# Kernel tuning notes

Measured on AMD Instinct MI355X. Metric: run time of the kernel, lower is better.

Reference implementation:

```python
import jax, jax.numpy as jnp
import numpy as np

B, T, D, H, NH = 128, 64, 64, 128, 4


def setup_inputs() -> dict:
    key = jax.random.key(0)
    ks = jax.random.split(key, 32)
    s = 0.05
    inp = {
        "x": jax.random.normal(ks[0], (B, T, D), dtype=jnp.float32),
        "mask": jnp.ones((B, T), dtype=jnp.int32),
        # per-feature GRU params (input size 1, PyTorch gate order r,z,n)
        "Wih": jax.random.normal(ks[1], (D, 3 * H), dtype=jnp.float32) * s,
        "Whh": jax.random.normal(ks[2], (D, 3 * H, H), dtype=jnp.float32) * s,
        "bih": jax.random.normal(ks[3], (D, 3 * H), dtype=jnp.float32) * s,
        "bhh": jax.random.normal(ks[4], (D, 3 * H), dtype=jnp.float32) * s,
        # MHA projections (stored [in,out]; y = x @ W + b)
        "Wq": jax.random.normal(ks[5], (H, H), dtype=jnp.float32) * s,
        "bq": jnp.zeros((H,), dtype=jnp.float32),
        "Wk": jax.random.normal(ks[6], (H, H), dtype=jnp.float32) * s,
        "bk": jnp.zeros((H,), dtype=jnp.float32),
        "Wv": jax.random.normal(ks[7], (H, H), dtype=jnp.float32) * s,
        "bv": jnp.zeros((H,), dtype=jnp.float32),
        "Wo": jax.random.normal(ks[8], (H, H), dtype=jnp.float32) * s,
        "bo": jnp.zeros((H,), dtype=jnp.float32),
        # FFN
        "W1": jax.random.normal(ks[9], (H, 2 * H), dtype=jnp.float32) * s,
        "b1": jnp.zeros((2 * H,), dtype=jnp.float32),
        "W2": jax.random.normal(ks[10], (2 * H, H), dtype=jnp.float32) * s,
        "b2": jnp.zeros((H,), dtype=jnp.float32),
        # LayerNorms
        "g1": jnp.ones((H,), dtype=jnp.float32),
        "be1": jnp.zeros((H,), dtype=jnp.float32),
        "g2": jnp.ones((H,), dtype=jnp.float32),
        "be2": jnp.zeros((H,), dtype=jnp.float32),
        # FinalAttentionQKV
        "Fq": jax.random.normal(ks[11], (H, H), dtype=jnp.float32) * s,
        "fbq": jnp.zeros((H,), dtype=jnp.float32),
        "Fk": jax.random.normal(ks[12], (H, H), dtype=jnp.float32) * s,
        "fbk": jnp.zeros((H,), dtype=jnp.float32),
        "Fv": jax.random.normal(ks[13], (H, H), dtype=jnp.float32) * s,
        "fbv": jnp.zeros((H,), dtype=jnp.float32),
        "Fout": jax.random.normal(ks[14], (H,), dtype=jnp.float32) * s,
        "fbout": jnp.zeros((), dtype=jnp.float32),
    }
    return inp


def _layernorm(x, g, b, eps=1e-5):
    m = jnp.mean(x, axis=-1, keepdims=True)
    v = jnp.mean((x - m) ** 2, axis=-1, keepdims=True)
    return (x - m) * jax.lax.rsqrt(v + eps) * g + b


def _forward(x, mask, Wih, Whh, bih, bhh, Wq, bq, Wk, bk, Wv, bv, Wo, bo,
             W1, b1, W2, b2, g1, be1, g2, be2,
             Fq, fbq, Fk, fbk, Fv, fbv, Fout, fbout):
    Bc, Tc, Dc = x.shape
    Hc = Whh.shape[-1]

    # --- D independent GRUs, fused: batch axes (B, D), scalar input per step ---
    def step(h, xt):  # h: [B,D,H], xt: [B,D]
        gx = xt[..., None] * Wih + bih                     # [B,D,3H]
        gh = jnp.einsum('bdh,dkh->bdk', h, Whh) + bhh      # [B,D,3H]
        r = jax.nn.sigmoid(gx[..., :Hc] + gh[..., :Hc])
        z = jax.nn.sigmoid(gx[..., Hc:2 * Hc] + gh[..., Hc:2 * Hc])
        n = jnp.tanh(gx[..., 2 * Hc:] + r * gh[..., 2 * Hc:])
        hn = (1.0 - z) * n + z * h
        return hn, hn

    xs = jnp.transpose(x, (1, 0, 2))                        # [T,B,D]
    h0 = jnp.zeros((Bc, Dc, Hc), dtype=x.dtype)
    _, ys = jax.lax.scan(step, h0, xs)                      # [T,B,D,H]

    # last_by_lengths: gather hidden state at index lengths-1 per batch element
    lengths = jnp.sum(mask, axis=1)                         # [B]
    idx = jnp.clip(lengths - 1, 0, Tc - 1)
    emb = ys[idx, jnp.arange(Bc)]                           # [B,D,H] (D tokens)

    # --- MHA (self-attention over D feature tokens); dropout = identity (eval) ---
    dk = Hc // NH
    def split_heads(t):
        return jnp.transpose(t.reshape(Bc, Dc, NH, dk), (0, 2, 1, 3))  # [B,NH,D,dk]
    q = split_heads(emb @ Wq + bq)
    k = split_heads(emb @ Wk + bk)
    v = split_heads(emb @ Wv + bv)
    scores = jnp.einsum('bhnd,bhmd->bhnm', q, k) / jnp.sqrt(jnp.float32(dk))
    attn = jax.nn.softmax(scores, axis=-1)
    o = jnp.einsum('bhnm,bhmd->bhnd', attn, v)
    o = jnp.transpose(o, (0, 2, 1, 3)).reshape(Bc, Dc, Hc)
    mha_out = o @ Wo + bo

    h1 = _layernorm(emb + mha_out, g1, be1)
    ffn = jax.nn.relu(h1 @ W1 + b1) @ W2 + b2
    h2 = _layernorm(h1 + ffn, g2, be2)

    # --- FinalAttentionQKV ---
    fq = (h2[:, -1, :] @ Fq + fbq)[:, None, :]              # [B,1,H]
    fk = h2 @ Fk + fbk                                      # [B,D,H]
    fv = h2 @ Fv + fbv                                      # [B,D,H]
    e = jnp.tanh(fq + fk) @ Fout + fbout                    # [B,D]
    a = jax.nn.softmax(e, axis=-1)
    return jnp.einsum('bn,bnh->bh', a, fv)                  # [B,H]


def reference(x, mask, Wih, Whh, bih, bhh, Wq, bq, Wk, bk, Wv, bv, Wo, bo,
              W1, b1, W2, b2, g1, be1, g2, be2,
              Fq, fbq, Fk, fbk, Fv, fbv, Fout, fbout):
    return _forward(x, mask, Wih, Whh, bih, bhh, Wq, bq, Wk, bk, Wv, bv, Wo, bo,
                    W1, b1, W2, b2, g1, be1, g2, be2,
                    Fq, fbq, Fk, fbk, Fv, fbv, Fout, fbout)
```

## Files before the change

### kernel.cpp

```cpp
#include <hip/hip_runtime.h>
#include <math.h>

#define BB 128
#define TT 64
#define DD 64
#define HH 128
#define NHH 4
#define K3H 384

typedef __attribute__((ext_vector_type(8))) short short8_t;
typedef __attribute__((ext_vector_type(4))) float float4_t;

#define LOG2E 1.4426950408889634f

__device__ __forceinline__ unsigned short f2bf(float f) {
    unsigned int u = __float_as_uint(f);
    u += 0x7fffu + ((u >> 16) & 1u);
    return (unsigned short)(u >> 16);
}

__device__ __forceinline__ unsigned pack_bf2(float lo, float hi) {
    return (unsigned)f2bf(lo) | ((unsigned)f2bf(hi) << 16);
}

__device__ __forceinline__ float bf2f(unsigned short s) {
    return __uint_as_float((unsigned)s << 16);
}

__global__ __launch_bounds__(512, 4) void gru_mfma_kernel(
    const float* __restrict__ x, const int* __restrict__ mask,
    const float* __restrict__ Wih, const float* __restrict__ Whh,
    const float* __restrict__ bih, const float* __restrict__ bhh,
    float* __restrict__ emb)
{
    const int d  = blockIdx.x;
    const int b0 = blockIdx.y * 16;
    const int tid = threadIdx.x;
    const int w = tid >> 6;
    const int l = tid & 63;
    const int m = l & 15;
    const int q = l >> 4;

    __shared__ __align__(16) unsigned short hbuf[2][16][136];
    __shared__ float xs_t[TT][16];
    __shared__ int tstar_s[16];

    for (int idx = tid; idx < 16 * TT; idx += 512) {
        int t = idx >> 4, row = idx & 15;
        xs_t[t][row] = x[((size_t)(b0 + row) * TT + t) * DD + d];
    }
    if (tid < 16) {
        int b = b0 + tid, len = 0;
        for (int t = 0; t < TT; ++t) len += mask[b * TT + t];
        int ts = len - 1;
        if (ts < 0) ts = 0;
        if (ts > TT - 1) ts = TT - 1;
        tstar_s[tid] = ts;
    }
    for (int idx = tid; idx < 16 * 136; idx += 512)
        ((unsigned short*)hbuf)[idx] = 0;

    short8_t Wf[3][4];
#pragma unroll
    for (int g = 0; g < 3; ++g) {
        float sc = (g == 2) ? (2.f * LOG2E) : (-LOG2E);
        int kcol = g * HH + 16 * w + m;
        const float* wrow = Whh + ((size_t)d * K3H + kcol) * HH;
#pragma unroll
        for (int kc = 0; kc < 4; ++kc) {
            int j0 = kc * 32 + q * 8;
            float4 w0 = *(const float4*)(wrow + j0);
            float4 w1 = *(const float4*)(wrow + j0 + 4);
            short8_t f;
            f[0] = (short)f2bf(w0.x * sc); f[1] = (short)f2bf(w0.y * sc);
            f[2] = (short)f2bf(w0.z * sc); f[3] = (short)f2bf(w0.w * sc);
            f[4] = (short)f2bf(w1.x * sc); f[5] = (short)f2bf(w1.y * sc);
            f[6] = (short)f2bf(w1.z * sc); f[7] = (short)f2bf(w1.w * sc);
            Wf[g][kc] = f;
        }
    }

    const int hcol0 = 16 * w + q * 4;
    float4 wr4 = *(const float4*)&Wih[d * K3H + hcol0];
    float4 wz4 = *(const float4*)&Wih[d * K3H + HH + hcol0];
    float4 wn4 = *(const float4*)&Wih[d * K3H + 2 * HH + hcol0];
    float4 br4 = *(const float4*)&bih[d * K3H + hcol0];
    float4 bz4 = *(const float4*)&bih[d * K3H + HH + hcol0];
    float4 bni4 = *(const float4*)&bih[d * K3H + 2 * HH + hcol0];
    float4 bhr4 = *(const float4*)&bhh[d * K3H + hcol0];
    float4 bhz4 = *(const float4*)&bhh[d * K3H + HH + hcol0];
    float4 bnh4 = *(const float4*)&bhh[d * K3H + 2 * HH + hcol0];
    float brs[4], bzs[4], bnis[4], bnhs[4], wrs[4], wzs[4], wns[4];
#pragma unroll
    for (int r = 0; r < 4; ++r) {
        wrs[r] = -LOG2E * ((const float*)&wr4)[r];
        wzs[r] = -LOG2E * ((const float*)&wz4)[r];
        wns[r] = 2.f * LOG2E * ((const float*)&wn4)[r];
        brs[r] = -LOG2E * (((const float*)&br4)[r] + ((const float*)&bhr4)[r]);
        bzs[r] = -LOG2E * (((const float*)&bz4)[r] + ((const float*)&bhz4)[r]);
        bnis[r] = 2.f * LOG2E * ((const float*)&bni4)[r];
        bnhs[r] = 2.f * LOG2E * ((const float*)&bnh4)[r];
    }

    float hprev[4];
#pragma unroll
    for (int i = 0; i < 4; ++i) hprev[i] = 0.f;

    __syncthreads();
    const int tstar_m = tstar_s[m];
    float* embp = emb + (((size_t)(b0 + m)) * DD + d) * HH + hcol0;

    for (int t = 0; t < TT; ++t) {
        const unsigned short* hb = &hbuf[t & 1][0][0];
        unsigned short* hbn = &hbuf[(t & 1) ^ 1][0][0];

        short8_t hf[4];
#pragma unroll
        for (int kc = 0; kc < 4; ++kc)
            hf[kc] = *(const short8_t*)(hb + m * 136 + kc * 32 + q * 8);
        float xv = xs_t[t][m];

        float4_t ar = {0.f,0.f,0.f,0.f}, az = {0.f,0.f,0.f,0.f}, an = {0.f,0.f,0.f,0.f};
#pragma unroll
        for (int kc = 0; kc < 4; ++kc) {
            ar = __builtin_amdgcn_mfma_f32_16x16x32_bf16(Wf[0][kc], hf[kc], ar, 0, 0, 0);
            az = __builtin_amdgcn_mfma_f32_16x16x32_bf16(Wf[1][kc], hf[kc], az, 0, 0, 0);
            an = __builtin_amdgcn_mfma_f32_16x16x32_bf16(Wf[2][kc], hf[kc], an, 0, 0, 0);
        }

        float hn4[4];
#pragma unroll
        for (int reg = 0; reg < 4; ++reg) {
            float grs = ar[reg] + fmaf(xv, wrs[reg], brs[reg]);
            float gzs = az[reg] + fmaf(xv, wzs[reg], bzs[reg]);
            float rg = __builtin_amdgcn_rcpf(1.f + __builtin_amdgcn_exp2f(grs));
            float zg = __builtin_amdgcn_rcpf(1.f + __builtin_amdgcn_exp2f(gzs));
            float gns = fmaf(rg, an[reg] + bnhs[reg], fmaf(xv, wns[reg], bnis[reg]));
            float tn = fmaf(-2.f, __builtin_amdgcn_rcpf(__builtin_amdgcn_exp2f(gns) + 1.f), 1.f);
            float hn = fmaf(zg, hprev[reg] - tn, tn);
            hprev[reg] = hn;
            hn4[reg] = hn;
        }
        uint2 uu;
        uu.x = pack_bf2(hn4[0], hn4[1]);
        uu.y = pack_bf2(hn4[2], hn4[3]);
        *(uint2*)(hbn + m * 136 + hcol0) = uu;
        if (t == tstar_m) {
            float4 hv; hv.x = hn4[0]; hv.y = hn4[1]; hv.z = hn4[2]; hv.w = hn4[3];
            *(float4*)embp = hv;
        }
        __syncthreads();
    }
}


__device__ __forceinline__ void load_wfrag(const float* __restrict__ Wp, int N,
                                           int col, float scale, int q,
                                           short8_t fr[4])
{
#pragma unroll
    for (int kc = 0; kc < 4; ++kc) {
        const float* p = Wp + (size_t)(kc * 32 + q * 8) * N + col;
        short8_t f;
#pragma unroll
        for (int j = 0; j < 8; ++j)
            f[j] = (short)f2bf(p[(size_t)j * N] * scale);
        fr[kc] = f;
    }
}

__device__ __forceinline__ void load_afrag(const unsigned short (*S)[136],
                                           short8_t Af[4][4], int m16, int q)
{
#pragma unroll
    for (int mt = 0; mt < 4; ++mt)
#pragma unroll
        for (int kc = 0; kc < 4; ++kc)
            Af[mt][kc] = *(const short8_t*)&S[mt * 16 + m16][kc * 32 + q * 8];
}

__device__ __forceinline__ void mm_regw(short8_t Af[4][4], short8_t Bf[4],
                                        float4_t acc[4])
{
#pragma unroll
    for (int mt = 0; mt < 4; ++mt) {
        float4_t a = acc[mt];
#pragma unroll
        for (int kc = 0; kc < 4; ++kc)
            a = __builtin_amdgcn_mfma_f32_16x16x32_bf16(Af[mt][kc], Bf[kc], a, 0, 0, 0);
        acc[mt] = a;
    }
}

__device__ __forceinline__ void zero4(float4_t acc[4]) {
#pragma unroll
    for (int mt = 0; mt < 4; ++mt) acc[mt] = (float4_t){0.f, 0.f, 0.f, 0.f};
}

__device__ __forceinline__ void store_rows(unsigned short (*Dst)[136], float4_t acc[4],
                                           float bv, int relu, int col, int q)
{
#pragma unroll
    for (int mt = 0; mt < 4; ++mt)
#pragma unroll
        for (int reg = 0; reg < 4; ++reg) {
            float v = acc[mt][reg] + bv;
            if (relu) v = fmaxf(v, 0.f);
            Dst[mt * 16 + q * 4 + reg][col] = f2bf(v);
        }
}

__global__ __launch_bounds__(512) void tail_kernel(
    const float* __restrict__ emb,
    const float* __restrict__ Wq, const float* __restrict__ bq,
    const float* __restrict__ Wk, const float* __restrict__ bk,
    const float* __restrict__ Wv, const float* __restrict__ bv,
    const float* __restrict__ Wo, const float* __restrict__ bo,
    const float* __restrict__ W1, const float* __restrict__ b1,
    const float* __restrict__ W2, const float* __restrict__ b2,
    const float* __restrict__ g1, const float* __restrict__ be1,
    const float* __restrict__ g2, const float* __restrict__ be2,
    const float* __restrict__ Fq, const float* __restrict__ fbq,
    const float* __restrict__ Fk, const float* __restrict__ fbk,
    const float* __restrict__ Fv, const float* __restrict__ fbv,
    const float* __restrict__ Fout, const float* __restrict__ fbout,
    float* __restrict__ out)
{
    const int b = blockIdx.x;
    const int tid = threadIdx.x;
    const int w = tid >> 6, l = tid & 63, m16 = l & 15, q = l >> 4;
    const int col = w * 16 + m16;

    __shared__ __align__(16) unsigned short E[64][136];
    __shared__ __align__(16) unsigned short Qs[64][136];
    __shared__ __align__(16) unsigned short Ks[64][136];
    __shared__ __align__(16) unsigned short Vt[128][72];
    __shared__ float sc4[4][64][66];
    __shared__ float lnp[64][8], lnp2[64][8];
    __shared__ float mean_s[64], rs_s[64];
    __shared__ float fq_s[128], fo_s[128], e_s[64], red_s[256];

    const float* embB = emb + (size_t)b * 64 * 128;
    const float SS = 0.17677669529663687f;

    short8_t WqF[4], WkF[4], WvF[4];
    load_wfrag(Wq, 128, col, SS, q, WqF);
    load_wfrag(Wk, 128, col, 1.f, q, WkF);
    load_wfrag(Wv, 128, col, 1.f, q, WvF);
    float bqv = bq[col] * SS, bkv = bk[col], bvv = bv[col];

    for (int it = tid; it < 2048; it += 512) {
        int r = it >> 5, c4 = (it & 31) << 2;
        float4 a = *(const float4*)&embB[r * 128 + c4];
        uint2 p; p.x = pack_bf2(a.x, a.y); p.y = pack_bf2(a.z, a.w);
        *(uint2*)&E[r][c4] = p;
    }
    __syncthreads();

    short8_t Af[4][4];
    float4_t acc[4];
    load_afrag(E, Af, m16, q);

    zero4(acc); mm_regw(Af, WqF, acc); store_rows(Qs, acc, bqv, 0, col, q);
    zero4(acc); mm_regw(Af, WkF, acc); store_rows(Ks, acc, bkv, 0, col, q);
    zero4(acc); mm_regw(Af, WvF, acc);
#pragma unroll
    for (int mt = 0; mt < 4; ++mt) {
        uint2 pk;
        pk.x = pack_bf2(acc[mt][0] + bvv, acc[mt][1] + bvv);
        pk.y = pack_bf2(acc[mt][2] + bvv, acc[mt][3] + bvv);
        *(uint2*)&Vt[col][mt * 16 + q * 4] = pk;
    }
    __syncthreads();

    short8_t WoF[4], W1aF[4], W1bF[4];
    load_wfrag(Wo, 128, col, 1.f, q, WoF);
    load_wfrag(W1, 256, col, 1.f, q, W1aF);
    load_wfrag(W1, 256, 128 + col, 1.f, q, W1bF);
    float bov = bo[col], b1a = b1[col], b1b = b1[128 + col];
    float g1v = g1[col], be1v = be1[col];

    {
        int hd = w >> 1, ntb = (w & 1) * 2;
#pragma unroll
        for (int mt = 0; mt < 4; ++mt) {
            short8_t Aq = *(const short8_t*)&Qs[mt * 16 + m16][hd * 32 + q * 8];
#pragma unroll
            for (int nn = 0; nn < 2; ++nn) {
                int nt = ntb + nn;
                short8_t Bk = *(const short8_t*)&Ks[nt * 16 + m16][hd * 32 + q * 8];
                float4_t a = {0.f, 0.f, 0.f, 0.f};
                a = __builtin_amdgcn_mfma_f32_16x16x32_bf16(Aq, Bk, a, 0, 0, 0);
#pragma unroll
                for (int reg = 0; reg < 4; ++reg)
                    sc4[hd][mt * 16 + q * 4 + reg][nt * 16 + m16] = a[reg];
            }
        }
    }
    __syncthreads();

    {
        int pr = tid >> 1, hd2 = pr >> 6, row = pr & 63, half = (tid & 1) * 32;
        float v[32]; float mx = -1e30f;
#pragma unroll
        for (int c = 0; c < 32; ++c) { v[c] = sc4[hd2][row][half + c]; mx = fmaxf(mx, v[c]); }
        mx = fmaxf(mx, __shfl_xor(mx, 1));
        float sum = 0.f;
#pragma unroll
        for (int c = 0; c < 32; ++c) { v[c] = __expf(v[c] - mx); sum += v[c]; }
        sum += __shfl_xor(sum, 1);
        float inv = __builtin_amdgcn_rcpf(sum);
        unsigned short (*Pd)[136] = (hd2 < 2) ? Qs : Ks;
        int cb = (hd2 & 1) * 64 + half;
#pragma unroll
        for (int c = 0; c < 16; ++c)
            *(unsigned*)&Pd[row][cb + 2 * c] = pack_bf2(v[2 * c] * inv, v[2 * c + 1] * inv);
    }
    __syncthreads();

    {
        int hd = w >> 1, nt = w & 1;
        const unsigned short (*P)[136] = (hd < 2) ? (const unsigned short (*)[136])Qs
                                                  : (const unsigned short (*)[136])Ks;
        int pb = (hd & 1) * 64;
        int vrow = hd * 32 + nt * 16 + m16;
        short8_t B0f = *(const short8_t*)&Vt[vrow][q * 8];
        short8_t B1f = *(const short8_t*)&Vt[vrow][32 + q * 8];
#pragma unroll
        for (int mt = 0; mt < 4; ++mt) {
            short8_t A0 = *(const short8_t*)&P[mt * 16 + m16][pb + q * 8];
            short8_t A1 = *(const short8_t*)&P[mt * 16 + m16][pb + 32 + q * 8];
            float4_t a = {0.f, 0.f, 0.f, 0.f};
            a = __builtin_amdgcn_mfma_f32_16x16x32_bf16(A0, B0f, a, 0, 0, 0);
            a = __builtin_amdgcn_mfma_f32_16x16x32_bf16(A1, B1f, a, 0, 0, 0);
#pragma unroll
            for (int reg = 0; reg < 4; ++reg)
                E[mt * 16 + q * 4 + reg][vrow] = f2bf(a[reg]);
        }
    }
    __syncthreads();

    short8_t W2aF[4], W2bF[4], FkF[4], FvF[4];
    load_wfrag(W2, 128, col, 1.f, q, W2aF);
    load_wfrag(W2 + (size_t)128 * 128, 128, col, 1.f, q, W2bF);
    load_wfrag(Fk, 128, col, 1.f, q, FkF);
    load_wfrag(Fv, 128, col, 1.f, q, FvF);
    float b2v = b2[col], fbkv = fbk[col], fbvv = fbv[col];
    float g2v = g2[col], be2v = be2[col];

    load_afrag(E, Af, m16, q);
    zero4(acc); mm_regw(Af, WoF, acc);
    float h1v[4][4];
#pragma unroll
    for (int mt = 0; mt < 4; ++mt)
#pragma unroll
        for (int reg = 0; reg < 4; ++reg) {
            int row = mt * 16 + q * 4 + reg;
            h1v[mt][reg] = acc[mt][reg] + bov + embB[(size_t)row * 128 + col];
        }
#pragma unroll
    for (int mt = 0; mt < 4; ++mt)
#pragma unroll
        for (int reg = 0; reg < 4; ++reg) {
            float s = h1v[mt][reg], s2 = s * s;
            s += __shfl_xor(s, 1); s += __shfl_xor(s, 2); s += __shfl_xor(s, 4); s += __shfl_xor(s, 8);
            s2 += __shfl_xor(s2, 1); s2 += __shfl_xor(s2, 2); s2 += __shfl_xor(s2, 4); s2 += __shfl_xor(s2, 8);
            if (m16 == 0) { int row = mt * 16 + q * 4 + reg; lnp[row][w] = s; lnp2[row][w] = s2; }
        }
    __syncthreads();
    if (tid < 64) {
        float s = 0.f, s2 = 0.f;
#pragma unroll
        for (int k = 0; k < 8; ++k) { s += lnp[tid][k]; s2 += lnp2[tid][k]; }
        float mn = s * (1.f / 128.f);
        mean_s[tid] = mn;
        rs_s[tid] = rsqrtf(s2 * (1.f / 128.f) - mn * mn + 1e-5f);
    }
    __syncthreads();
#pragma unroll
    for (int mt = 0; mt < 4; ++mt)
#pragma unroll
        for (int reg = 0; reg < 4; ++reg) {
            int row = mt * 16 + q * 4 + reg;
            float hv = (h1v[mt][reg] - mean_s[row]) * rs_s[row] * g1v + be1v;
            h1v[mt][reg] = hv;
            E[row][col] = f2bf(hv);
        }
    __syncthreads();

    load_afrag(E, Af, m16, q);
    zero4(acc); mm_regw(Af, W1aF, acc); store_rows(Qs, acc, b1a, 1, col, q);
    zero4(acc); mm_regw(Af, W1bF, acc); store_rows(Ks, acc, b1b, 1, col, q);
    __syncthreads();

    {
        short8_t AfQ[4][4], AfK[4][4];
        load_afrag(Qs, AfQ, m16, q);
        load_afrag(Ks, AfK, m16, q);
        zero4(acc); mm_regw(AfQ, W2aF, acc); mm_regw(AfK, W2bF, acc);
    }
#pragma unroll
    for (int mt = 0; mt < 4; ++mt)
#pragma unroll
        for (int reg = 0; reg < 4; ++reg)
            h1v[mt][reg] = acc[mt][reg] + b2v + h1v[mt][reg];
#pragma unroll
    for (int mt = 0; mt < 4; ++mt)
#pragma unroll
        for (int reg = 0; reg < 4; ++reg) {
            float s = h1v[mt][reg], s2 = s * s;
            s += __shfl_xor(s, 1); s += __shfl_xor(s, 2); s += __shfl_xor(s, 4); s += __shfl_xor(s, 8);
            s2 += __shfl_xor(s2, 1); s2 += __shfl_xor(s2, 2); s2 += __shfl_xor(s2, 4); s2 += __shfl_xor(s2, 8);
            if (m16 == 0) { int row = mt * 16 + q * 4 + reg; lnp[row][w] = s; lnp2[row][w] = s2; }
        }
    __syncthreads();
    if (tid < 64) {
        float s = 0.f, s2 = 0.f;
#pragma unroll
        for (int k = 0; k < 8; ++k) { s += lnp[tid][k]; s2 += lnp2[tid][k]; }
        float mn = s * (1.f / 128.f);
        mean_s[tid] = mn;
        rs_s[tid] = rsqrtf(s2 * (1.f / 128.f) - mn * mn + 1e-5f);
    }
    __syncthreads();
#pragma unroll
    for (int mt = 0; mt < 4; ++mt)
#pragma unroll
        for (int reg = 0; reg < 4; ++reg) {
            int row = mt * 16 + q * 4 + reg;
            float hv = (h1v[mt][reg] - mean_s[row]) * rs_s[row] * g2v + be2v;
            E[row][col] = f2bf(hv);
        }
    __syncthreads();

    load_afrag(E, Af, m16, q);
    zero4(acc); mm_regw(Af, FkF, acc); store_rows(Qs, acc, fbkv, 0, col, q);
    zero4(acc); mm_regw(Af, FvF, acc); store_rows(Ks, acc, fbvv, 0, col, q);
    if (tid < 128) {
        fo_s[tid] = Fout[tid];
        float a = fbq[tid];
        for (int mm2 = 0; mm2 < 128; ++mm2)
            a = fmaf(bf2f(E[63][mm2]), Fq[mm2 * 128 + tid], a);
        fq_s[tid] = a;
    }
    __syncthreads();

    {
        int dd = tid >> 3, c8 = tid & 7;
        float p = 0.f;
#pragma unroll
        for (int c = 0; c < 16; ++c) {
            int cc = c8 * 16 + c;
            float t = fq_s[cc] + bf2f(Qs[dd][cc]);
            float tn = 1.f - 2.f * __builtin_amdgcn_rcpf(
                __builtin_amdgcn_exp2f(2.f * LOG2E * t) + 1.f);
            p = fmaf(tn, fo_s[cc], p);
        }
        p += __shfl_xor(p, 1); p += __shfl_xor(p, 2); p += __shfl_xor(p, 4);
        if (c8 == 0) e_s[dd] = p + fbout[0];
    }
    __syncthreads();
    if (tid < 64) {
        float e = e_s[tid], mx = e;
        for (int o = 32; o; o >>= 1) mx = fmaxf(mx, __shfl_xor(mx, o));
        float pe = __expf(e - mx);
        float s = pe;
        for (int o = 32; o; o >>= 1) s += __shfl_xor(s, o);
        e_s[tid] = pe / s;
    }
    __syncthreads();
    if (tid < 256) {
        int c2 = tid & 127, rg2 = tid >> 7;
        float a = 0.f;
        for (int d2 = rg2 * 32; d2 < rg2 * 32 + 32; ++d2)
            a = fmaf(e_s[d2], bf2f(Ks[d2][c2]), a);
        red_s[tid] = a;
    }
    __syncthreads();
    if (tid < 128)
        out[(size_t)b * 128 + tid] = red_s[tid] + red_s[tid + 128];
}

extern "C" void kernel_launch(void* const* d_in, const int* in_sizes, int n_in,
                              void* d_out, int out_size, void* d_ws, size_t ws_size,
                              hipStream_t stream)
{
    const float* x    = (const float*)d_in[0];
    const int*   mask = (const int*)d_in[1];
    const float* Wih  = (const float*)d_in[2];
    const float* Whh  = (const float*)d_in[3];
    const float* bih  = (const float*)d_in[4];
    const float* bhh  = (const float*)d_in[5];
    const float* Wq = (const float*)d_in[6];   const float* bq = (const float*)d_in[7];
    const float* Wk = (const float*)d_in[8];   const float* bk = (const float*)d_in[9];
    const float* Wv = (const float*)d_in[10];  const float* bv = (const float*)d_in[11];
    const float* Wo = (const float*)d_in[12];  const float* bo = (const float*)d_in[13];
    const float* W1 = (const float*)d_in[14];  const float* b1 = (const float*)d_in[15];
    const float* W2 = (const float*)d_in[16];  const float* b2 = (const float*)d_in[17];
    const float* g1 = (const float*)d_in[18];  const float* be1 = (const float*)d_in[19];
    const float* g2 = (const float*)d_in[20];  const float* be2 = (const float*)d_in[21];
    const float* Fq = (const float*)d_in[22];  const float* fbq = (const float*)d_in[23];
    const float* Fk = (const float*)d_in[24];  const float* fbk = (const float*)d_in[25];
    const float* Fv = (const float*)d_in[26];  const float* fbv = (const float*)d_in[27];
    const float* Fout = (const float*)d_in[28]; const float* fbout = (const float*)d_in[29];
    float* out = (float*)d_out;
    float* ws  = (float*)d_ws;

    float* emb = ws;

    gru_mfma_kernel<<<dim3(DD, BB / 16), 512, 0, stream>>>(x, mask, Wih, Whh, bih, bhh, emb);
    tail_kernel<<<BB, 512, 0, stream>>>(
        emb, Wq, bq, Wk, bk, Wv, bv, Wo, bo, W1, b1, W2, b2,
        g1, be1, g2, be2, Fq, fbq, Fk, fbk, Fv, fbv, Fout, fbout, out);
}
```

Measured before the change: 250.9 us.

## Split tail kernel across two blocks per batch and add final reduce kernel

The tail kernel now runs two blocks per batch element. Each block recomputes K and V for all 64 rows but handles Q, attention, Wo, FFN, LayerNorms and the Fk/Fv projections for only its 32 rows. Fk, Fv and the last-row Fq projection go to workspace, and a new third kernel computes the final tanh-attention softmax and weighted sum. The GRU loop also seeds the MFMA accumulators with the hidden-path biases and uses the hardware bf16 pack intrinsic. This doubles the tail's parallelism and cuts shared memory per block, at the cost of redundant K/V work, global round-trips and an extra launch.

```diff
diff --git a/kernel.cpp b/kernel.cpp
--- a/kernel.cpp
+++ b/kernel.cpp
@@ -1,4 +1,5 @@
 #include <hip/hip_runtime.h>
+#include <hip/hip_bf16.h>
 #include <math.h>
 
 #define BB 128
@@ -21,6 +22,13 @@
 
 __device__ __forceinline__ unsigned pack_bf2(float lo, float hi) {
     return (unsigned)f2bf(lo) | ((unsigned)f2bf(hi) << 16);
+}
+
+__device__ __forceinline__ unsigned pack_bf2_hw(float lo, float hi) {
+    __hip_bfloat162 p = __float22bfloat162_rn(make_float2(lo, hi));
+    unsigned u;
+    __builtin_memcpy(&u, &p, 4);
+    return u;
 }
 
 __device__ __forceinline__ float bf2f(unsigned short s) {
@@ -120,7 +128,9 @@
             hf[kc] = *(const short8_t*)(hb + m * 136 + kc * 32 + q * 8);
         float xv = xs_t[t][m];
 
-        float4_t ar = {0.f,0.f,0.f,0.f}, az = {0.f,0.f,0.f,0.f}, an = {0.f,0.f,0.f,0.f};
+        float4_t ar = {brs[0], brs[1], brs[2], brs[3]};
+        float4_t az = {bzs[0], bzs[1], bzs[2], bzs[3]};
+        float4_t an = {bnhs[0], bnhs[1], bnhs[2], bnhs[3]};
 #pragma unroll
         for (int kc = 0; kc < 4; ++kc) {
             ar = __builtin_amdgcn_mfma_f32_16x16x32_bf16(Wf[0][kc], hf[kc], ar, 0, 0, 0);
@@ -131,19 +141,19 @@
         float hn4[4];
 #pragma unroll
         for (int reg = 0; reg < 4; ++reg) {
-            float grs = ar[reg] + fmaf(xv, wrs[reg], brs[reg]);
-            float gzs = az[reg] + fmaf(xv, wzs[reg], bzs[reg]);
+            float grs = fmaf(xv, wrs[reg], ar[reg]);
+            float gzs = fmaf(xv, wzs[reg], az[reg]);
             float rg = __builtin_amdgcn_rcpf(1.f + __builtin_amdgcn_exp2f(grs));
             float zg = __builtin_amdgcn_rcpf(1.f + __builtin_amdgcn_exp2f(gzs));
-            float gns = fmaf(rg, an[reg] + bnhs[reg], fmaf(xv, wns[reg], bnis[reg]));
+            float gns = fmaf(rg, an[reg], fmaf(xv, wns[reg], bnis[reg]));
             float tn = fmaf(-2.f, __builtin_amdgcn_rcpf(__builtin_amdgcn_exp2f(gns) + 1.f), 1.f);
             float hn = fmaf(zg, hprev[reg] - tn, tn);
             hprev[reg] = hn;
             hn4[reg] = hn;
         }
         uint2 uu;
-        uu.x = pack_bf2(hn4[0], hn4[1]);
-        uu.y = pack_bf2(hn4[2], hn4[3]);
+        uu.x = pack_bf2_hw(hn4[0], hn4[1]);
+        uu.y = pack_bf2_hw(hn4[2], hn4[3]);
         *(uint2*)(hbn + m * 136 + hcol0) = uu;
         if (t == tstar_m) {
             float4 hv; hv.x = hn4[0]; hv.y = hn4[1]; hv.z = hn4[2]; hv.w = hn4[3];
@@ -167,47 +177,6 @@
             f[j] = (short)f2bf(p[(size_t)j * N] * scale);
         fr[kc] = f;
     }
-}
-
-__device__ __forceinline__ void load_afrag(const unsigned short (*S)[136],
-                                           short8_t Af[4][4], int m16, int q)
-{
-#pragma unroll
-    for (int mt = 0; mt < 4; ++mt)
-#pragma unroll
-        for (int kc = 0; kc < 4; ++kc)
-            Af[mt][kc] = *(const short8_t*)&S[mt * 16 + m16][kc * 32 + q * 8];
-}
-
-__device__ __forceinline__ void mm_regw(short8_t Af[4][4], short8_t Bf[4],
-                                        float4_t acc[4])
-{
-#pragma unroll
-    for (int mt = 0; mt < 4; ++mt) {
-        float4_t a = acc[mt];
-#pragma unroll
-        for (int kc = 0; kc < 4; ++kc)
-            a = __builtin_amdgcn_mfma_f32_16x16x32_bf16(Af[mt][kc], Bf[kc], a, 0, 0, 0);
-        acc[mt] = a;
-    }
-}
-
-__device__ __forceinline__ void zero4(float4_t acc[4]) {
-#pragma unroll
-    for (int mt = 0; mt < 4; ++mt) acc[mt] = (float4_t){0.f, 0.f, 0.f, 0.f};
-}
-
-__device__ __forceinline__ void store_rows(unsigned short (*Dst)[136], float4_t acc[4],
-                                           float bv, int relu, int col, int q)
-{
-#pragma unroll
-    for (int mt = 0; mt < 4; ++mt)
-#pragma unroll
-        for (int reg = 0; reg < 4; ++reg) {
-            float v = acc[mt][reg] + bv;
-            if (relu) v = fmaxf(v, 0.f);
-            Dst[mt * 16 + q * 4 + reg][col] = f2bf(v);
-        }
 }
 
 __global__ __launch_bounds__(512) void tail_kernel(
@@ -223,10 +192,11 @@
     const float* __restrict__ Fq, const float* __restrict__ fbq,
     const float* __restrict__ Fk, const float* __restrict__ fbk,
     const float* __restrict__ Fv, const float* __restrict__ fbv,
-    const float* __restrict__ Fout, const float* __restrict__ fbout,
-    float* __restrict__ out)
+    float* __restrict__ fkb, float* __restrict__ fvb, float* __restrict__ fqb)
 {
-    const int b = blockIdx.x;
+    const int b = blockIdx.x >> 1;
+    const int half = blockIdx.x & 1;
+    const int r0 = half * 32;
     const int tid = threadIdx.x;
     const int w = tid >> 6, l = tid & 63, m16 = l & 15, q = l >> 4;
     const int col = w * 16 + m16;
@@ -235,10 +205,9 @@
     __shared__ __align__(16) unsigned short Qs[64][136];
     __shared__ __align__(16) unsigned short Ks[64][136];
     __shared__ __align__(16) unsigned short Vt[128][72];
-    __shared__ float sc4[4][64][66];
-    __shared__ float lnp[64][8], lnp2[64][8];
-    __shared__ float mean_s[64], rs_s[64];
-    __shared__ float fq_s[128], fo_s[128], e_s[64], red_s[256];
+    __shared__ float sc4[4][32][66];
+    __shared__ float lnp[32][8], lnp2[32][8];
+    __shared__ float mean_s[32], rs_s[32];
 
     const float* embB = emb + (size_t)b * 64 * 128;
     const float SS = 0.17677669529663687f;
@@ -257,19 +226,49 @@
     }
     __syncthreads();
 
-    short8_t Af[4][4];
-    float4_t acc[4];
-    load_afrag(E, Af, m16, q);
-
-    zero4(acc); mm_regw(Af, WqF, acc); store_rows(Qs, acc, bqv, 0, col, q);
-    zero4(acc); mm_regw(Af, WkF, acc); store_rows(Ks, acc, bkv, 0, col, q);
-    zero4(acc); mm_regw(Af, WvF, acc);
-#pragma unroll
-    for (int mt = 0; mt < 4; ++mt) {
-        uint2 pk;
-        pk.x = pack_bf2(acc[mt][0] + bvv, acc[mt][1] + bvv);
-        pk.y = pack_bf2(acc[mt][2] + bvv, acc[mt][3] + bvv);
-        *(uint2*)&Vt[col][mt * 16 + q * 4] = pk;
+    short8_t Af4[4][4];
+#pragma unroll
+    for (int mt = 0; mt < 4; ++mt)
+#pragma unroll
+        for (int kc = 0; kc < 4; ++kc)
+            Af4[mt][kc] = *(const short8_t*)&E[mt * 16 + m16][kc * 32 + q * 8];
+
+    {
+        float4_t a4[4];
+#pragma unroll
+        for (int mt = 0; mt < 4; ++mt) {
+            float4_t a = {0.f, 0.f, 0.f, 0.f};
+#pragma unroll
+            for (int kc = 0; kc < 4; ++kc)
+                a = __builtin_amdgcn_mfma_f32_16x16x32_bf16(Af4[mt][kc], WkF[kc], a, 0, 0, 0);
+            a4[mt] = a;
+        }
+#pragma unroll
+        for (int mt = 0; mt < 4; ++mt)
+#pragma unroll
+            for (int reg = 0; reg < 4; ++reg)
+                Ks[mt * 16 + q * 4 + reg][col] = f2bf(a4[mt][reg] + bkv);
+#pragma unroll
+        for (int mt = 0; mt < 4; ++mt) {
+            float4_t a = {0.f, 0.f, 0.f, 0.f};
+#pragma unroll
+            for (int kc = 0; kc < 4; ++kc)
+                a = __builtin_amdgcn_mfma_f32_16x16x32_bf16(Af4[mt][kc], WvF[kc], a, 0, 0, 0);
+            uint2 pk;
+            pk.x = pack_bf2(a[0] + bvv, a[1] + bvv);
+            pk.y = pack_bf2(a[2] + bvv, a[3] + bvv);
+            *(uint2*)&Vt[col][mt * 16 + q * 4] = pk;
+        }
+#pragma unroll
+        for (int mt = 0; mt < 2; ++mt) {
+            float4_t a = {0.f, 0.f, 0.f, 0.f};
+#pragma unroll
+            for (int kc = 0; kc < 4; ++kc)
+                a = __builtin_amdgcn_mfma_f32_16x16x32_bf16(Af4[half * 2 + mt][kc], WqF[kc], a, 0, 0, 0);
+#pragma unroll
+            for (int reg = 0; reg < 4; ++reg)
+                Qs[r0 + mt * 16 + q * 4 + reg][col] = f2bf(a[reg] + bqv);
+        }
     }
     __syncthreads();
 
@@ -283,8 +282,8 @@
     {
         int hd = w >> 1, ntb = (w & 1) * 2;
 #pragma unroll
-        for (int mt = 0; mt < 4; ++mt) {
-            short8_t Aq = *(const short8_t*)&Qs[mt * 16 + m16][hd * 32 + q * 8];
+        for (int mt = 0; mt < 2; ++mt) {
+            short8_t Aq = *(const short8_t*)&Qs[r0 + mt * 16 + m16][hd * 32 + q * 8];
 #pragma unroll
             for (int nn = 0; nn < 2; ++nn) {
                 int nt = ntb + nn;
@@ -300,42 +299,41 @@
     __syncthreads();
 
     {
-        int pr = tid >> 1, hd2 = pr >> 6, row = pr & 63, half = (tid & 1) * 32;
-        float v[32]; float mx = -1e30f;
-#pragma unroll
-        for (int c = 0; c < 32; ++c) { v[c] = sc4[hd2][row][half + c]; mx = fmaxf(mx, v[c]); }
+        int pr = tid >> 2, sub = tid & 3;
+        int hd2 = pr >> 5, row = pr & 31;
+        float v[16]; float mx = -1e30f;
+#pragma unroll
+        for (int c = 0; c < 16; ++c) { v[c] = sc4[hd2][row][sub * 16 + c]; mx = fmaxf(mx, v[c]); }
         mx = fmaxf(mx, __shfl_xor(mx, 1));
+        mx = fmaxf(mx, __shfl_xor(mx, 2));
         float sum = 0.f;
 #pragma unroll
-        for (int c = 0; c < 32; ++c) { v[c] = __expf(v[c] - mx); sum += v[c]; }
-        sum += __shfl_xor(sum, 1);
+        for (int c = 0; c < 16; ++c) { v[c] = __expf(v[c] - mx); sum += v[c]; }
+        sum += __shfl_xor(sum, 1); sum += __shfl_xor(sum, 2);
         float inv = __builtin_amdgcn_rcpf(sum);
-        unsigned short (*Pd)[136] = (hd2 < 2) ? Qs : Ks;
-        int cb = (hd2 & 1) * 64 + half;
-#pragma unroll
-        for (int c = 0; c < 16; ++c)
-            *(unsigned*)&Pd[row][cb + 2 * c] = pack_bf2(v[2 * c] * inv, v[2 * c + 1] * inv);
+        int prow = (hd2 >> 1) * 32 + row, pc = (hd2 & 1) * 64 + sub * 16;
+#pragma unroll
+        for (int c = 0; c < 8; ++c)
+            *(unsigned*)&Qs[prow][pc + 2 * c] = pack_bf2(v[2 * c] * inv, v[2 * c + 1] * inv);
     }
     __syncthreads();
 
     {
-        int hd = w >> 1, nt = w & 1;
-        const unsigned short (*P)[136] = (hd < 2) ? (const unsigned short (*)[136])Qs
-                                                  : (const unsigned short (*)[136])Ks;
-        int pb = (hd & 1) * 64;
-        int vrow = hd * 32 + nt * 16 + m16;
+        int hd = w >> 1, ntv = w & 1;
+        int vrow = hd * 32 + ntv * 16 + m16;
         short8_t B0f = *(const short8_t*)&Vt[vrow][q * 8];
         short8_t B1f = *(const short8_t*)&Vt[vrow][32 + q * 8];
-#pragma unroll
-        for (int mt = 0; mt < 4; ++mt) {
-            short8_t A0 = *(const short8_t*)&P[mt * 16 + m16][pb + q * 8];
-            short8_t A1 = *(const short8_t*)&P[mt * 16 + m16][pb + 32 + q * 8];
+        int prow0 = (hd >> 1) * 32, pc = (hd & 1) * 64;
+#pragma unroll
+        for (int mt = 0; mt < 2; ++mt) {
+            short8_t A0 = *(const short8_t*)&Qs[prow0 + mt * 16 + m16][pc + q * 8];
+            short8_t A1 = *(const short8_t*)&Qs[prow0 + mt * 16 + m16][pc + 32 + q * 8];
             float4_t a = {0.f, 0.f, 0.f, 0.f};
             a = __builtin_amdgcn_mfma_f32_16x16x32_bf16(A0, B0f, a, 0, 0, 0);
             a = __builtin_amdgcn_mfma_f32_16x16x32_bf16(A1, B1f, a, 0, 0, 0);
 #pragma unroll
             for (int reg = 0; reg < 4; ++reg)
-                E[mt * 16 + q * 4 + reg][vrow] = f2bf(a[reg]);
+                E[r0 + mt * 16 + q * 4 + reg][vrow] = f2bf(a[reg]);
         }
     }
     __syncthreads();
@@ -348,27 +346,36 @@
     float b2v = b2[col], fbkv = fbk[col], fbvv = fbv[col];
     float g2v = g2[col], be2v = be2[col];
 
-    load_afrag(E, Af, m16, q);
-    zero4(acc); mm_regw(Af, WoF, acc);
-    float h1v[4][4];
-#pragma unroll
-    for (int mt = 0; mt < 4; ++mt)
-#pragma unroll
-        for (int reg = 0; reg < 4; ++reg) {
-            int row = mt * 16 + q * 4 + reg;
-            h1v[mt][reg] = acc[mt][reg] + bov + embB[(size_t)row * 128 + col];
-        }
-#pragma unroll
-    for (int mt = 0; mt < 4; ++mt)
+    short8_t Af2[2][4];
+#pragma unroll
+    for (int mt = 0; mt < 2; ++mt)
+#pragma unroll
+        for (int kc = 0; kc < 4; ++kc)
+            Af2[mt][kc] = *(const short8_t*)&E[r0 + mt * 16 + m16][kc * 32 + q * 8];
+    float h1v[2][4];
+#pragma unroll
+    for (int mt = 0; mt < 2; ++mt) {
+        float4_t a = {0.f, 0.f, 0.f, 0.f};
+#pragma unroll
+        for (int kc = 0; kc < 4; ++kc)
+            a = __builtin_amdgcn_mfma_f32_16x16x32_bf16(Af2[mt][kc], WoF[kc], a, 0, 0, 0);
+#pragma unroll
+        for (int reg = 0; reg < 4; ++reg) {
+            int row = r0 + mt * 16 + q * 4 + reg;
+            h1v[mt][reg] = a[reg] + bov + embB[(size_t)row * 128 + col];
+        }
+    }
+#pragma unroll
+    for (int mt = 0; mt < 2; ++mt)
 #pragma unroll
         for (int reg = 0; reg < 4; ++reg) {
             float s = h1v[mt][reg], s2 = s * s;
             s += __shfl_xor(s, 1); s += __shfl_xor(s, 2); s += __shfl_xor(s, 4); s += __shfl_xor(s, 8);
             s2 += __shfl_xor(s2, 1); s2 += __shfl_xor(s2, 2); s2 += __shfl_xor(s2, 4); s2 += __shfl_xor(s2, 8);
-            if (m16 == 0) { int row = mt * 16 + q * 4 + reg; lnp[row][w] = s; lnp2[row][w] = s2; }
-        }
-    __syncthreads();
-    if (tid < 64) {
+            if (m16 == 0) { int lr = mt * 16 + q * 4 + reg; lnp[lr][w] = s; lnp2[lr][w] = s2; }
+        }
+    __syncthreads();
+    if (tid < 32) {
         float s = 0.f, s2 = 0.f;
 #pragma unroll
         for (int k = 0; k < 8; ++k) { s += lnp[tid][k]; s2 += lnp2[tid][k]; }
@@ -378,43 +385,66 @@
     }
     __syncthreads();
 #pragma unroll
-    for (int mt = 0; mt < 4; ++mt)
-#pragma unroll
-        for (int reg = 0; reg < 4; ++reg) {
-            int row = mt * 16 + q * 4 + reg;
-            float hv = (h1v[mt][reg] - mean_s[row]) * rs_s[row] * g1v + be1v;
+    for (int mt = 0; mt < 2; ++mt)
+#pragma unroll
+        for (int reg = 0; reg < 4; ++reg) {
+            int lr = mt * 16 + q * 4 + reg;
+            float hv = (h1v[mt][reg] - mean_s[lr]) * rs_s[lr] * g1v + be1v;
             h1v[mt][reg] = hv;
-            E[row][col] = f2bf(hv);
-        }
-    __syncthreads();
-
-    load_afrag(E, Af, m16, q);
-    zero4(acc); mm_regw(Af, W1aF, acc); store_rows(Qs, acc, b1a, 1, col, q);
-    zero4(acc); mm_regw(Af, W1bF, acc); store_rows(Ks, acc, b1b, 1, col, q);
-    __syncthreads();
-
-    {
-        short8_t AfQ[4][4], AfK[4][4];
-        load_afrag(Qs, AfQ, m16, q);
-        load_afrag(Ks, AfK, m16, q);
-        zero4(acc); mm_regw(AfQ, W2aF, acc); mm_regw(AfK, W2bF, acc);
-    }
-#pragma unroll
-    for (int mt = 0; mt < 4; ++mt)
+            E[r0 + lr][col] = f2bf(hv);
+        }
+    __syncthreads();
+
+#pragma unroll
+    for (int mt = 0; mt < 2; ++mt)
+#pragma unroll
+        for (int kc = 0; kc < 4; ++kc)
+            Af2[mt][kc] = *(const short8_t*)&E[r0 + mt * 16 + m16][kc * 32 + q * 8];
+#pragma unroll
+    for (int mt = 0; mt < 2; ++mt) {
+        float4_t a = {0.f, 0.f, 0.f, 0.f}, c2 = {0.f, 0.f, 0.f, 0.f};
+#pragma unroll
+        for (int kc = 0; kc < 4; ++kc) {
+            a  = __builtin_amdgcn_mfma_f32_16x16x32_bf16(Af2[mt][kc], W1aF[kc], a, 0, 0, 0);
+            c2 = __builtin_amdgcn_mfma_f32_16x16x32_bf16(Af2[mt][kc], W1bF[kc], c2, 0, 0, 0);
+        }
+#pragma unroll
+        for (int reg = 0; reg < 4; ++reg) {
+            int row = r0 + mt * 16 + q * 4 + reg;
+            Qs[row][col] = f2bf(fmaxf(a[reg] + b1a, 0.f));
+            Ks[row][col] = f2bf(fmaxf(c2[reg] + b1b, 0.f));
+        }
+    }
+    __syncthreads();
+
+#pragma unroll
+    for (int mt = 0; mt < 2; ++mt) {
+        float4_t a = {0.f, 0.f, 0.f, 0.f};
+#pragma unroll
+        for (int kc = 0; kc < 4; ++kc) {
+            short8_t AQ = *(const short8_t*)&Qs[r0 + mt * 16 + m16][kc * 32 + q * 8];
+            a = __builtin_amdgcn_mfma_f32_16x16x32_bf16(AQ, W2aF[kc], a, 0, 0, 0);
+        }
+#pragma unroll
+        for (int kc = 0; kc < 4; ++kc) {
+            short8_t AK = *(const short8_t*)&Ks[r0 + mt * 16 + m16][kc * 32 + q * 8];
+            a = __builtin_amdgcn_mfma_f32_16x16x32_bf16(AK, W2bF[kc], a, 0, 0, 0);
+        }
 #pragma unroll
         for (int reg = 0; reg < 4; ++reg)
-            h1v[mt][reg] = acc[mt][reg] + b2v + h1v[mt][reg];
-#pragma unroll
-    for (int mt = 0; mt < 4; ++mt)
+            h1v[mt][reg] = a[reg] + b2v + h1v[mt][reg];
+    }
+#pragma unroll
+    for (int mt = 0; mt < 2; ++mt)
 #pragma unroll
         for (int reg = 0; reg < 4; ++reg) {
             float s = h1v[mt][reg], s2 = s * s;
             s += __shfl_xor(s, 1); s += __shfl_xor(s, 2); s += __shfl_xor(s, 4); s += __shfl_xor(s, 8);
             s2 += __shfl_xor(s2, 1); s2 += __shfl_xor(s2, 2); s2 += __shfl_xor(s2, 4); s2 += __shfl_xor(s2, 8);
-            if (m16 == 0) { int row = mt * 16 + q * 4 + reg; lnp[row][w] = s; lnp2[row][w] = s2; }
-        }
-    __syncthreads();
-    if (tid < 64) {
+            if (m16 == 0) { int lr = mt * 16 + q * 4 + reg; lnp[lr][w] = s; lnp2[lr][w] = s2; }
+        }
+    __syncthreads();
+    if (tid < 32) {
         float s = 0.f, s2 = 0.f;
 #pragma unroll
         for (int k = 0; k < 8; ++k) { s += lnp[tid][k]; s2 += lnp2[tid][k]; }
@@ -424,41 +454,70 @@
     }
     __syncthreads();
 #pragma unroll
-    for (int mt = 0; mt < 4; ++mt)
-#pragma unroll
-        for (int reg = 0; reg < 4; ++reg) {
-            int row = mt * 16 + q * 4 + reg;
-            float hv = (h1v[mt][reg] - mean_s[row]) * rs_s[row] * g2v + be2v;
-            E[row][col] = f2bf(hv);
-        }
-    __syncthreads();
-
-    load_afrag(E, Af, m16, q);
-    zero4(acc); mm_regw(Af, FkF, acc); store_rows(Qs, acc, fbkv, 0, col, q);
-    zero4(acc); mm_regw(Af, FvF, acc); store_rows(Ks, acc, fbvv, 0, col, q);
-    if (tid < 128) {
+    for (int mt = 0; mt < 2; ++mt)
+#pragma unroll
+        for (int reg = 0; reg < 4; ++reg) {
+            int lr = mt * 16 + q * 4 + reg;
+            float hv = (h1v[mt][reg] - mean_s[lr]) * rs_s[lr] * g2v + be2v;
+            E[r0 + lr][col] = f2bf(hv);
+        }
+    __syncthreads();
+
+#pragma unroll
+    for (int mt = 0; mt < 2; ++mt)
+#pragma unroll
+        for (int kc = 0; kc < 4; ++kc)
+            Af2[mt][kc] = *(const short8_t*)&E[r0 + mt * 16 + m16][kc * 32 + q * 8];
+#pragma unroll
+    for (int mt = 0; mt < 2; ++mt) {
+        float4_t a = {0.f, 0.f, 0.f, 0.f}, c2 = {0.f, 0.f, 0.f, 0.f};
+#pragma unroll
+        for (int kc = 0; kc < 4; ++kc) {
+            a  = __builtin_amdgcn_mfma_f32_16x16x32_bf16(Af2[mt][kc], FkF[kc], a, 0, 0, 0);
+            c2 = __builtin_amdgcn_mfma_f32_16x16x32_bf16(Af2[mt][kc], FvF[kc], c2, 0, 0, 0);
+        }
+#pragma unroll
+        for (int reg = 0; reg < 4; ++reg) {
+            int row = r0 + mt * 16 + q * 4 + reg;
+            fkb[((size_t)b * DD + row) * HH + col] = a[reg] + fbkv;
+            fvb[((size_t)b * DD + row) * HH + col] = c2[reg] + fbvv;
+        }
+    }
+    if (half == 1) {
+        int co = tid >> 2, sub = tid & 3;
+        float acc = 0.f;
+#pragma unroll 8
+        for (int mm2 = sub * 32; mm2 < sub * 32 + 32; ++mm2)
+            acc = fmaf(bf2f(E[63][mm2]), Fq[(size_t)mm2 * 128 + co], acc);
+        acc += __shfl_xor(acc, 1);
+        acc += __shfl_xor(acc, 2);
+        if (sub == 0) fqb[(size_t)b * 128 + co] = acc + fbq[co];
+    }
+}
+
+__global__ __launch_bounds__(256) void final_reduce_kernel(
+    const float* __restrict__ fqb, const float* __restrict__ fkb,
+    const float* __restrict__ fvb, const float* __restrict__ Fout,
+    const float* __restrict__ fbout, float* __restrict__ out)
+{
+    int b = blockIdx.x;
+    int tid = threadIdx.x;
+    __shared__ float fq_s[HH], fo_s[HH], e_s[DD];
+    __shared__ float red_s[256];
+    if (tid < HH) {
+        fq_s[tid] = fqb[(size_t)b * HH + tid];
         fo_s[tid] = Fout[tid];
-        float a = fbq[tid];
-        for (int mm2 = 0; mm2 < 128; ++mm2)
-            a = fmaf(bf2f(E[63][mm2]), Fq[mm2 * 128 + tid], a);
-        fq_s[tid] = a;
-    }
-    __syncthreads();
-
-    {
-        int dd = tid >> 3, c8 = tid & 7;
-        float p = 0.f;
-#pragma unroll
-        for (int c = 0; c < 16; ++c) {
-            int cc = c8 * 16 + c;
-            float t = fq_s[cc] + bf2f(Qs[dd][cc]);
-            float tn = 1.f - 2.f * __builtin_amdgcn_rcpf(
-                __builtin_amdgcn_exp2f(2.f * LOG2E * t) + 1.f);
-            p = fmaf(tn, fo_s[cc], p);
-        }
-        p += __shfl_xor(p, 1); p += __shfl_xor(p, 2); p += __shfl_xor(p, 4);
-        if (c8 == 0) e_s[dd] = p + fbout[0];
-    }
+    }
+    __syncthreads();
+    int dd = tid >> 2, sub = tid & 3;
+    const float* fkrow = fkb + ((size_t)b * DD + dd) * HH + sub * 32;
+    float p = 0.f;
+#pragma unroll 8
+    for (int mm = 0; mm < 32; ++mm)
+        p = fmaf(tanhf(fq_s[sub * 32 + mm] + fkrow[mm]), fo_s[sub * 32 + mm], p);
+    p += __shfl_xor(p, 1);
+    p += __shfl_xor(p, 2);
+    if (sub == 0) e_s[dd] = p + fbout[0];
     __syncthreads();
     if (tid < 64) {
         float e = e_s[tid], mx = e;
@@ -469,16 +528,14 @@
         e_s[tid] = pe / s;
     }
     __syncthreads();
-    if (tid < 256) {
-        int c2 = tid & 127, rg2 = tid >> 7;
-        float a = 0.f;
-        for (int d2 = rg2 * 32; d2 < rg2 * 32 + 32; ++d2)
-            a = fmaf(e_s[d2], bf2f(Ks[d2][c2]), a);
-        red_s[tid] = a;
-    }
-    __syncthreads();
-    if (tid < 128)
-        out[(size_t)b * 128 + tid] = red_s[tid] + red_s[tid + 128];
+    int col = tid & 127, rg = tid >> 7;
+    float acc = 0.f;
+    for (int d2 = rg * 32; d2 < rg * 32 + 32; ++d2)
+        acc = fmaf(e_s[d2], fvb[((size_t)b * DD + d2) * HH + col], acc);
+    red_s[tid] = acc;
+    __syncthreads();
+    if (rg == 0)
+        out[(size_t)b * HH + col] = red_s[col] + red_s[col + 128];
 }
 
 extern "C" void kernel_launch(void* const* d_in, const int* in_sizes, int n_in,
@@ -507,9 +564,13 @@
     float* ws  = (float*)d_ws;
 
     float* emb = ws;
+    float* fkb = ws + 1048576;
+    float* fvb = ws + 2097152;
+    float* fqb = ws + 3145728;
 
     gru_mfma_kernel<<<dim3(DD, BB / 16), 512, 0, stream>>>(x, mask, Wih, Whh, bih, bhh, emb);
-    tail_kernel<<<BB, 512, 0, stream>>>(
+    tail_kernel<<<BB * 2, 512, 0, stream>>>(
         emb, Wq, bq, Wk, bk, Wv, bv, Wo, bo, W1, b1, W2, b2,
-        g1, be1, g2, be2, Fq, fbq, Fk, fbk, Fv, fbv, Fout, fbout, out);
-}
+        g1, be1, g2, be2, Fq, fbq, Fk, fbk, Fv, fbv, fkb, fvb, fqb);
+    final_reduce_kernel<<<BB, 256, 0, stream>>>(fqb, fkb, fvb, Fout, fbout, out);
+}
```

Result: no change. 251.6 us (+0.3%).
